# Optimization experiments

Hardware: AMD Instinct MI355X
Metric: run time of the kernel (lower is better)

The kernel has to match this reference:

```python
import jax, jax.numpy as jnp
import numpy as np

# arch config (matches init_kwargs)
T = 8
G = 16
D = 64
GG = G * G
THR = 0.5            # arch.object_threshold
Z_COS_MATCH_W = 5.0  # arch.z_cos_match_weight
ADJ_W = 1.0
PRES_W = 1.0
POOL_W = 1.0
OBJ_W = 10.0
FLOW_W = 1.0
FULL_OBJ = 200000.0  # arch.full_object_weight
FLOW_END = 100000.0  # arch.flow_cooling_end_step


def setup_inputs() -> dict:
    key = jax.random.key(0)
    k1, k2, k3 = jax.random.split(key, 3)
    B = 128
    return {
        "z_what": jax.random.normal(k1, (T * B, GG, D), dtype=jnp.float32),
        "z_pres_prob": jax.random.uniform(k2, (T * B, GG, 1), dtype=jnp.float32),
        "grid_flow": jax.random.uniform(k3, (T * B, GG, 1), dtype=jnp.float32),
        "global_step": 50000,
    }


def _maxpool3x3(x):
    # x: (N, C, G, G); torch MaxPool2d(3, stride=1, padding=1) pads with -inf
    return jax.lax.reduce_window(
        x, -jnp.inf, jax.lax.max,
        window_dimensions=(1, 1, 3, 3), window_strides=(1, 1, 1, 1),
        padding=[(0, 0), (0, 0), (1, 1), (1, 1)])


def reference(z_what, z_pres_prob, grid_flow, global_step):
    B = z_what.shape[0] // T
    zw = z_what.reshape(T, B, GG, D)
    zp = z_pres_prob.reshape(T, B, GG, 1)

    # ---- z_what_loss_grid_cell: adjacent squared deltas ----
    z_what_loss = jnp.sum((zw[1:] - zw[:-1]) ** 2)

    # ---- z_pres_loss_grid_cell ----
    sim = 1.0 - (zp[2:] - zp[:-2]) ** 2
    deltas = (zp[2:] - zp[1:-1]) ** 2 + (zp[:-2] - zp[1:-1]) ** 2
    z_pres_loss = jnp.sum(sim * deltas)

    # ---- z_what_consistency_pool (cosine_sim branch) ----
    w = jnp.abs(zw) * zp                                    # (T,B,GG,D)
    wi = w.transpose(0, 1, 3, 2).reshape(T * B, D, G, G)
    smoothed = _maxpool3x3(wi).reshape(T, B, D, GG).transpose(0, 1, 3, 2)
    dot = jnp.sum(smoothed[:-1] * w[1:], axis=-1)           # (T-1,B,GG)
    na = jnp.maximum(jnp.sqrt(jnp.sum(smoothed[:-1] ** 2, -1)), 1e-6)
    nb = jnp.maximum(jnp.sqrt(jnp.sum(w[1:] ** 2, -1)), 1e-6)
    cos_pool = dot / (na * nb)
    pw = zp[..., 0]
    pw = (pw[:-1] + pw[1:]) * 0.5                           # (T-1,B,GG)
    z_what_loss_pool = -jnp.sum(cos_pool * pw)

    # ---- z_what_consistency_objects (vectorized over objects) ----
    # For every active cell (t,b,i,j) at time t<T-1, compare its z_what (prior)
    # with z_what at t+1 over the 3x3 circular neighborhood, restricted to
    # neighbor cells whose z_pres > threshold. Loss per object:
    #   -z_cos_match_weight * max(sim) + sum(sim); skipped if no active neighbor.
    zpg = zp.reshape(T, B, G, G)
    zwg = zw.reshape(T, B, G, G, D)
    prior = zwg[:-1]                                        # (T-1,B,G,G,D)
    prior_n = jnp.maximum(jnp.sqrt(jnp.sum(prior ** 2, -1)), 1e-8)
    pres_prior = zpg[:-1] > THR                             # (T-1,B,G,G)
    sum_sim = jnp.zeros(prior.shape[:-1], dtype=prior.dtype)
    max_sim = jnp.full(prior.shape[:-1], -jnp.inf, dtype=prior.dtype)
    has_nb = jnp.zeros(prior.shape[:-1], dtype=bool)
    for di in (-1, 0, 1):
        for dj in (-1, 0, 1):
            nbw = jnp.roll(zwg[1:], (-di, -dj), axis=(2, 3))       # circular
            nbp = jnp.roll(zpg[1:], (-di, -dj), axis=(2, 3)) > THR
            dotn = jnp.sum(prior * nbw, axis=-1)
            nn = jnp.maximum(jnp.sqrt(jnp.sum(nbw ** 2, -1)), 1e-8)
            s = dotn / (prior_n * nn)
            sum_sim = sum_sim + jnp.where(nbp, s, 0.0)
            max_sim = jnp.maximum(max_sim, jnp.where(nbp, s, -jnp.inf))
            has_nb = has_nb | nbp
    valid = pres_prior & has_nb
    contrib = jnp.where(valid, -Z_COS_MATCH_W * max_sim + sum_sim, 0.0)
    z_what_loss_objects = jnp.sum(contrib)
    objects_detected = jnp.sum(pres_prior.astype(jnp.int32))

    # ---- compute_flow_loss ----
    zp_img = z_pres_prob.reshape(-1, 1, G, G)
    zp_max = _maxpool3x3(zp_img).reshape(-1, GG, 1)
    flow = grid_flow.reshape(-1, GG, 1)
    fmask = flow > 0.5
    flow_loss = jnp.sum(jnp.where(fmask, (zp_max - flow) ** 2, 0.0)) \
        + 100.0 * jnp.maximum(0.0, jnp.sum(zp_img) - jnp.sum(flow))

    # ---- total (Space base loss excluded; external submodule) ----
    scale_obj = min(1.0, float(global_step) / FULL_OBJ)
    scale_flow = max(0.0, 1.0 - float(global_step) / FLOW_END)
    loss = (z_what_loss * ADJ_W
            + z_pres_loss * PRES_W
            + z_what_loss_pool * POOL_W
            + z_what_loss_objects * scale_obj * OBJ_W
            + flow_loss * FLOW_W * scale_flow)
    return loss
```

## Files before the change

kernel.cpp:

```cpp
#include <hip/hip_runtime.h>
#include <math.h>

#define TT 8
#define BB 128
#define GG 256
#define DD 64
#define NCH 4
#define CF4 4
#define ST 5
#define NPAIR ((TT - 1) * BB)


__device__ inline float wred(float v) {
#pragma unroll
    for (int off = 32; off > 0; off >>= 1) v += __shfl_xor(v, off, 64);
    return v;
}
__device__ inline float dot4(float4 a, float4 b) {
    return a.x * b.x + a.y * b.y + a.z * b.z + a.w * b.w;
}
__device__ inline float4 fabs4(float4 a) {
    return make_float4(fabsf(a.x), fabsf(a.y), fabsf(a.z), fabsf(a.w));
}
__device__ inline float4 max4(float4 a, float4 b) {
    return make_float4(fmaxf(a.x, b.x), fmaxf(a.y, b.y), fmaxf(a.z, b.z), fmaxf(a.w, b.w));
}
__device__ inline float4 scale4(float4 a, float s) {
    return make_float4(a.x * s, a.y * s, a.z * s, a.w * s);
}
__device__ inline float4 sub4(float4 a, float4 b) {
    return make_float4(a.x - b.x, a.y - b.y, a.z - b.z, a.w - b.w);
}
__device__ inline float4 shfl4(float4 v, int src) {
    return make_float4(__shfl(v.x, src, 64), __shfl(v.y, src, 64),
                       __shfl(v.z, src, 64), __shfl(v.w, src, 64));
}

__global__ __launch_bounds__(256) void pair_kernel(const float* __restrict__ zw,
                                                   const float* __restrict__ zp,
                                                   const float* __restrict__ flow,
                                                   float* __restrict__ part) {
    const int pairIdx = blockIdx.x;
    const int t = pairIdx >> 7;
    const int b = pairIdx & (BB - 1);
    const int tid = threadIdx.x;
    const int gi = tid >> 4, gj = tid & 15;
    const int lane = tid & 63;

    __shared__ float4 shB[GG * ST];
    __shared__ float4 shR[GG * ST];
    __shared__ float pA[GG], pB[GG], nB[GG];
    __shared__ float bred[8][4];

    const float4* gA = (const float4*)zw + (size_t)(t * BB + b) * 1024;
    const float4* gB = gA + (size_t)BB * 1024;

    const float pAc = zp[(size_t)(t * BB + b) * GG + tid];
    const float pBc = zp[(size_t)((t + 1) * BB + b) * GG + tid];
    const float f = flow[(size_t)(t * BB + b) * GG + tid];
    float f7 = 0.f, pC = 0.f;
    if (t == 6) f7 = flow[(size_t)(7 * BB + b) * GG + tid];
    if (t <= 5) pC = zp[(size_t)((t + 2) * BB + b) * GG + tid];
    pA[tid] = pAc;
    pB[tid] = pBc;

    int nbc[9];
    unsigned inbM = 0;
    {
        int m = 0;
#pragma unroll
        for (int di = -1; di <= 1; di++) {
#pragma unroll
            for (int dj = -1; dj <= 1; dj++) {
                nbc[m] = (((gi + di) & 15) << 4) | ((gj + dj) & 15);
                if (((unsigned)(gi + di) < 16u) && ((unsigned)(gj + dj) < 16u))
                    inbM |= (1u << m);
                m++;
            }
        }
    }

    float zdiff = 0.f, sa = 0.f, sb = 0.f, poolDot = 0.f, poolN = 0.f;
    float dots[9] = {0.f, 0.f, 0.f, 0.f, 0.f, 0.f, 0.f, 0.f, 0.f};

    float4 cA[CF4], cB[CF4];
#pragma unroll
    for (int q = 0; q < CF4; q++) {
        cA[q] = gA[tid * 16 + q];
        cB[q] = gB[tid * 16 + q];
    }

#pragma unroll 1
    for (int c = 0; c < NCH; c++) {
        float4 nA4[CF4], nB4[CF4];
        if (c + 1 < NCH) {
#pragma unroll
            for (int q = 0; q < CF4; q++) {
                nA4[q] = gA[tid * 16 + (c + 1) * CF4 + q];
                nB4[q] = gB[tid * 16 + (c + 1) * CF4 + q];
            }
        }

#pragma unroll
        for (int q = 0; q < CF4; q++) {
            float4 d = sub4(cB[q], cA[q]);
            zdiff += dot4(d, d);
            sa += dot4(cA[q], cA[q]);
            sb += dot4(cB[q], cB[q]);
            dots[4] += dot4(cA[q], cB[q]);
            float4 wa = scale4(fabs4(cA[q]), pAc);
            float4 rm = wa;
            float4 lft = shfl4(wa, lane - 1);
            if (gj > 0) rm = max4(rm, lft);
            float4 rgt = shfl4(wa, lane + 1);
            if (gj < 15) rm = max4(rm, rgt);
            shB[tid * ST + q] = cB[q];
            shR[tid * ST + q] = rm;
        }
        __syncthreads();

#pragma unroll
        for (int k = 0; k < 9; k++) {
            if (k == 4) continue;
            int base = nbc[k] * ST;
#pragma unroll
            for (int q = 0; q < CF4; q++) dots[k] += dot4(cA[q], shB[base + q]);
        }
#pragma unroll
        for (int q = 0; q < CF4; q++) {
            float4 sm = shR[tid * ST + q];
            if (gi > 0) sm = max4(sm, shR[(tid - 16) * ST + q]);
            if (gi < 15) sm = max4(sm, shR[(tid + 16) * ST + q]);
            poolDot += dot4(sm, fabs4(cB[q]));
            poolN += dot4(sm, sm);
        }
        __syncthreads();

        if (c + 1 < NCH) {
#pragma unroll
            for (int q = 0; q < CF4; q++) { cA[q] = nA4[q]; cB[q] = nB4[q]; }
        }
    }

    nB[tid] = sqrtf(sb);
    __syncthreads();

    float prior_n = fmaxf(sqrtf(sa), 1e-8f);
    float sum_sim = 0.f, max_sim = -1e30f;
    bool has = false;
#pragma unroll
    for (int k = 0; k < 9; k++) {
        float nn = fmaxf(nB[nbc[k]], 1e-8f);
        float s = dots[k] / (prior_n * nn);
        if (pB[nbc[k]] > 0.5f) {
            sum_sim += s;
            max_sim = fmaxf(max_sim, s);
            has = true;
        }
    }
    float obj = ((pAc > 0.5f) && has) ? (sum_sim - 5.0f * max_sim) : 0.f;

    float na_pool = fmaxf(sqrtf(poolN), 1e-6f);
    float nb_pool = fmaxf(pBc * sqrtf(sb), 1e-6f);
    float poolc = -(pBc * poolDot) / (na_pool * nb_pool) * 0.5f * (pAc + pBc);

    float mx = pAc;
#pragma unroll
    for (int k = 0; k < 9; k++)
        if (k != 4 && ((inbM >> k) & 1u)) mx = fmaxf(mx, pA[nbc[k]]);
    float fsq = 0.f;
    if (f > 0.5f) { float d = mx - f; fsq = d * d; }
    float szp = pAc, sflow = f;
    if (t == 6) {
        float mxB = pBc;
#pragma unroll
        for (int k = 0; k < 9; k++)
            if (k != 4 && ((inbM >> k) & 1u)) mxB = fmaxf(mxB, pB[nbc[k]]);
        if (f7 > 0.5f) { float d = mxB - f7; fsq += d * d; }
        szp += pBc;
        sflow += f7;
    }

    float pres = 0.f;
    if (t <= 5) {
        float s02 = pC - pAc;
        float sim = 1.f - s02 * s02;
        float d2 = pC - pBc, d0 = pAc - pBc;
        pres = sim * (d2 * d2 + d0 * d0);
    }

    float r[7] = {zdiff, pres, poolc, obj, fsq, szp, sflow};
    int w = tid >> 6;
#pragma unroll
    for (int j = 0; j < 7; j++) {
        float rv = wred(r[j]);
        if (lane == 0) bred[j][w] = rv;
    }
    __syncthreads();
    if (tid < 7)
        part[pairIdx * 8 + tid] = bred[tid][0] + bred[tid][1] + bred[tid][2] + bred[tid][3];
}

__global__ __launch_bounds__(256) void final_kernel(const float* __restrict__ part,
                                                    const int* __restrict__ gs,
                                                    float* __restrict__ out) {
    const int tid = threadIdx.x;
    __shared__ float bred[7][4];
    float c[7] = {0.f, 0.f, 0.f, 0.f, 0.f, 0.f, 0.f};
    for (int p = tid; p < NPAIR; p += 256) {
        const float* r = part + p * 8;
#pragma unroll
        for (int j = 0; j < 7; j++) c[j] += r[j];
    }
    int w = tid >> 6, lane = tid & 63;
#pragma unroll
    for (int j = 0; j < 7; j++) {
        float rv = wred(c[j]);
        if (lane == 0) bred[j][w] = rv;
    }
    __syncthreads();
    if (tid == 0) {
        float s[7];
#pragma unroll
        for (int j = 0; j < 7; j++) s[j] = bred[j][0] + bred[j][1] + bred[j][2] + bred[j][3];
        float step = (float)gs[0];
        float scale_obj = fminf(1.f, step / 200000.f);
        float scale_flow = fmaxf(0.f, 1.f - step / 100000.f);
        float flow_loss = s[4] + 100.f * fmaxf(0.f, s[5] - s[6]);
        out[0] = s[0]
               + s[1]
               + s[2]
               + s[3] * scale_obj * 10.0f
               + flow_loss * scale_flow;
    }
}

extern "C" void kernel_launch(void* const* d_in, const int* in_sizes, int n_in,
                              void* d_out, int out_size, void* d_ws, size_t ws_size,
                              hipStream_t stream) {
    const float* zw = (const float*)d_in[0];
    const float* zp = (const float*)d_in[1];
    const float* fl = (const float*)d_in[2];
    const int* gs = (const int*)d_in[3];
    float* ws = (float*)d_ws;

    pair_kernel<<<NPAIR, 256, 0, stream>>>(zw, zp, fl, ws);
    final_kernel<<<1, 256, 0, stream>>>(ws, gs, (float*)d_out);
}
```

Measured before the change: 158.2 us.

## Split each frame pair into two half-grid blocks with halo rows

Each (t,b) pair is now handled by two 128-thread blocks, each covering 8 grid rows plus two halo rows. Halo threads reload the neighbouring rows' z_what and recompute their row-max and norms. One shared buffer is reused for the B features and the pool row-max, which adds an extra barrier per chunk. The register prefetch of the next chunk is dropped. The aim is more, smaller blocks and lower shared memory per block for better occupancy, at the cost of about 25% redundant halo loads and more synchronisation.

```diff
diff --git a/kernel.cpp b/kernel.cpp
--- a/kernel.cpp
+++ b/kernel.cpp
@@ -9,6 +9,8 @@
 #define CF4 4
 #define ST 5
 #define NPAIR ((TT - 1) * BB)
+#define NBLK (NPAIR * 2)
+#define LROWS 10
 
 
 __device__ inline float wred(float v) {
@@ -36,35 +38,53 @@
                        __shfl(v.z, src, 64), __shfl(v.w, src, 64));
 }
 
-__global__ __launch_bounds__(256) void pair_kernel(const float* __restrict__ zw,
+__global__ __launch_bounds__(128) void pair_kernel(const float* __restrict__ zw,
                                                    const float* __restrict__ zp,
                                                    const float* __restrict__ flow,
                                                    float* __restrict__ part) {
-    const int pairIdx = blockIdx.x;
+    const int blk = blockIdx.x;
+    const int pairIdx = blk >> 1;
+    const int half = blk & 1;
     const int t = pairIdx >> 7;
     const int b = pairIdx & (BB - 1);
+    const int r0 = half << 3;
     const int tid = threadIdx.x;
-    const int gi = tid >> 4, gj = tid & 15;
+    const int gj = tid & 15;
+    const int grow = r0 + (tid >> 4);
+    const int lr = (tid >> 4) + 1;
+    const int cell = (grow << 4) | gj;
     const int lane = tid & 63;
 
-    __shared__ float4 shB[GG * ST];
-    __shared__ float4 shR[GG * ST];
-    __shared__ float pA[GG], pB[GG], nB[GG];
-    __shared__ float bred[8][4];
+    const bool isHalo = (tid < 32);
+    const int hs = (tid < 16) ? 0 : 9;
+    const int hrow = (r0 - 1 + hs) & 15;
+    const int hcell = (hrow << 4) | gj;
+
+    __shared__ float4 shS[LROWS * 16 * ST];
+    __shared__ float pAloc[LROWS * 16], pBloc[LROWS * 16], nBloc[LROWS * 16];
+    __shared__ float bred[7][2];
 
     const float4* gA = (const float4*)zw + (size_t)(t * BB + b) * 1024;
     const float4* gB = gA + (size_t)BB * 1024;
-
-    const float pAc = zp[(size_t)(t * BB + b) * GG + tid];
-    const float pBc = zp[(size_t)((t + 1) * BB + b) * GG + tid];
-    const float f = flow[(size_t)(t * BB + b) * GG + tid];
+    const float* zpA = zp + (size_t)(t * BB + b) * GG;
+    const float* zpB = zp + (size_t)((t + 1) * BB + b) * GG;
+
+    const float pAc = zpA[cell];
+    const float pBc = zpB[cell];
+    pAloc[lr * 16 + gj] = pAc;
+    pBloc[lr * 16 + gj] = pBc;
+    float pAh = 0.f;
+    if (isHalo) {
+        pAh = zpA[hcell];
+        pAloc[hs * 16 + gj] = pAh;
+        pBloc[hs * 16 + gj] = zpB[hcell];
+    }
+    const float f = flow[(size_t)(t * BB + b) * GG + cell];
     float f7 = 0.f, pC = 0.f;
-    if (t == 6) f7 = flow[(size_t)(7 * BB + b) * GG + tid];
-    if (t <= 5) pC = zp[(size_t)((t + 2) * BB + b) * GG + tid];
-    pA[tid] = pAc;
-    pB[tid] = pBc;
-
-    int nbc[9];
+    if (t == 6) f7 = flow[(size_t)(7 * BB + b) * GG + cell];
+    if (t <= 5) pC = zp[(size_t)((t + 2) * BB + b) * GG + cell];
+
+    int nbl[9];
     unsigned inbM = 0;
     {
         int m = 0;
@@ -72,35 +92,41 @@
         for (int di = -1; di <= 1; di++) {
 #pragma unroll
             for (int dj = -1; dj <= 1; dj++) {
-                nbc[m] = (((gi + di) & 15) << 4) | ((gj + dj) & 15);
-                if (((unsigned)(gi + di) < 16u) && ((unsigned)(gj + dj) < 16u))
+                nbl[m] = (lr + di) * 16 + ((gj + dj) & 15);
+                if (((unsigned)(grow + di) < 16u) && ((unsigned)(gj + dj) < 16u))
                     inbM |= (1u << m);
                 m++;
             }
         }
     }
-
-    float zdiff = 0.f, sa = 0.f, sb = 0.f, poolDot = 0.f, poolN = 0.f;
+    __syncthreads();
+
+    float zdiff = 0.f, sa = 0.f, sb = 0.f, hsb = 0.f, poolDot = 0.f, poolN = 0.f;
     float dots[9] = {0.f, 0.f, 0.f, 0.f, 0.f, 0.f, 0.f, 0.f, 0.f};
-
-    float4 cA[CF4], cB[CF4];
-#pragma unroll
-    for (int q = 0; q < CF4; q++) {
-        cA[q] = gA[tid * 16 + q];
-        cB[q] = gB[tid * 16 + q];
-    }
 
 #pragma unroll 1
     for (int c = 0; c < NCH; c++) {
-        float4 nA4[CF4], nB4[CF4];
-        if (c + 1 < NCH) {
+        float4 cA[CF4], cB[CF4], rm[CF4], hrm[CF4];
+#pragma unroll
+        for (int q = 0; q < CF4; q++) {
+            cA[q] = gA[cell * 16 + c * CF4 + q];
+            cB[q] = gB[cell * 16 + c * CF4 + q];
+        }
+        float4 hB4[CF4];
+        if (isHalo) {
 #pragma unroll
             for (int q = 0; q < CF4; q++) {
-                nA4[q] = gA[tid * 16 + (c + 1) * CF4 + q];
-                nB4[q] = gB[tid * 16 + (c + 1) * CF4 + q];
+                float4 hA4 = gA[hcell * 16 + c * CF4 + q];
+                hB4[q] = gB[hcell * 16 + c * CF4 + q];
+                hsb += dot4(hB4[q], hB4[q]);
+                float4 wa = scale4(fabs4(hA4), pAh);
+                hrm[q] = wa;
+                float4 lft = shfl4(wa, lane - 1);
+                if (gj > 0) hrm[q] = max4(hrm[q], lft);
+                float4 rgt = shfl4(wa, lane + 1);
+                if (gj < 15) hrm[q] = max4(hrm[q], rgt);
             }
         }
-
 #pragma unroll
         for (int q = 0; q < CF4; q++) {
             float4 d = sub4(cB[q], cA[q]);
@@ -109,40 +135,50 @@
             sb += dot4(cB[q], cB[q]);
             dots[4] += dot4(cA[q], cB[q]);
             float4 wa = scale4(fabs4(cA[q]), pAc);
-            float4 rm = wa;
+            rm[q] = wa;
             float4 lft = shfl4(wa, lane - 1);
-            if (gj > 0) rm = max4(rm, lft);
+            if (gj > 0) rm[q] = max4(rm[q], lft);
             float4 rgt = shfl4(wa, lane + 1);
-            if (gj < 15) rm = max4(rm, rgt);
-            shB[tid * ST + q] = cB[q];
-            shR[tid * ST + q] = rm;
+            if (gj < 15) rm[q] = max4(rm[q], rgt);
+            shS[(lr * 16 + gj) * ST + q] = cB[q];
+        }
+        if (isHalo) {
+#pragma unroll
+            for (int q = 0; q < CF4; q++) shS[(hs * 16 + gj) * ST + q] = hB4[q];
         }
         __syncthreads();
 
 #pragma unroll
         for (int k = 0; k < 9; k++) {
             if (k == 4) continue;
-            int base = nbc[k] * ST;
-#pragma unroll
-            for (int q = 0; q < CF4; q++) dots[k] += dot4(cA[q], shB[base + q]);
-        }
+            int base = nbl[k] * ST;
+#pragma unroll
+            for (int q = 0; q < CF4; q++) dots[k] += dot4(cA[q], shS[base + q]);
+        }
+        __syncthreads();
+
+#pragma unroll
+        for (int q = 0; q < CF4; q++) shS[(lr * 16 + gj) * ST + q] = rm[q];
+        if (isHalo) {
+#pragma unroll
+            for (int q = 0; q < CF4; q++) shS[(hs * 16 + gj) * ST + q] = hrm[q];
+        }
+        __syncthreads();
+
+        const bool up = (grow > 0), dn = (grow < 15);
 #pragma unroll
         for (int q = 0; q < CF4; q++) {
-            float4 sm = shR[tid * ST + q];
-            if (gi > 0) sm = max4(sm, shR[(tid - 16) * ST + q]);
-            if (gi < 15) sm = max4(sm, shR[(tid + 16) * ST + q]);
+            float4 sm = rm[q];
+            if (up) sm = max4(sm, shS[((lr - 1) * 16 + gj) * ST + q]);
+            if (dn) sm = max4(sm, shS[((lr + 1) * 16 + gj) * ST + q]);
             poolDot += dot4(sm, fabs4(cB[q]));
             poolN += dot4(sm, sm);
         }
         __syncthreads();
-
-        if (c + 1 < NCH) {
-#pragma unroll
-            for (int q = 0; q < CF4; q++) { cA[q] = nA4[q]; cB[q] = nB4[q]; }
-        }
-    }
-
-    nB[tid] = sqrtf(sb);
+    }
+
+    nBloc[lr * 16 + gj] = sqrtf(sb);
+    if (isHalo) nBloc[hs * 16 + gj] = sqrtf(hsb);
     __syncthreads();
 
     float prior_n = fmaxf(sqrtf(sa), 1e-8f);
@@ -150,9 +186,9 @@
     bool has = false;
 #pragma unroll
     for (int k = 0; k < 9; k++) {
-        float nn = fmaxf(nB[nbc[k]], 1e-8f);
+        float nn = fmaxf(nBloc[nbl[k]], 1e-8f);
         float s = dots[k] / (prior_n * nn);
-        if (pB[nbc[k]] > 0.5f) {
+        if (pBloc[nbl[k]] > 0.5f) {
             sum_sim += s;
             max_sim = fmaxf(max_sim, s);
             has = true;
@@ -167,7 +203,7 @@
     float mx = pAc;
 #pragma unroll
     for (int k = 0; k < 9; k++)
-        if (k != 4 && ((inbM >> k) & 1u)) mx = fmaxf(mx, pA[nbc[k]]);
+        if (k != 4 && ((inbM >> k) & 1u)) mx = fmaxf(mx, pAloc[nbl[k]]);
     float fsq = 0.f;
     if (f > 0.5f) { float d = mx - f; fsq = d * d; }
     float szp = pAc, sflow = f;
@@ -175,7 +211,7 @@
         float mxB = pBc;
 #pragma unroll
         for (int k = 0; k < 9; k++)
-            if (k != 4 && ((inbM >> k) & 1u)) mxB = fmaxf(mxB, pB[nbc[k]]);
+            if (k != 4 && ((inbM >> k) & 1u)) mxB = fmaxf(mxB, pBloc[nbl[k]]);
         if (f7 > 0.5f) { float d = mxB - f7; fsq += d * d; }
         szp += pBc;
         sflow += f7;
@@ -198,7 +234,7 @@
     }
     __syncthreads();
     if (tid < 7)
-        part[pairIdx * 8 + tid] = bred[tid][0] + bred[tid][1] + bred[tid][2] + bred[tid][3];
+        part[blk * 8 + tid] = bred[tid][0] + bred[tid][1];
 }
 
 __global__ __launch_bounds__(256) void final_kernel(const float* __restrict__ part,
@@ -207,7 +243,7 @@
     const int tid = threadIdx.x;
     __shared__ float bred[7][4];
     float c[7] = {0.f, 0.f, 0.f, 0.f, 0.f, 0.f, 0.f};
-    for (int p = tid; p < NPAIR; p += 256) {
+    for (int p = tid; p < NBLK; p += 256) {
         const float* r = part + p * 8;
 #pragma unroll
         for (int j = 0; j < 7; j++) c[j] += r[j];
@@ -244,6 +280,6 @@
     const int* gs = (const int*)d_in[3];
     float* ws = (float*)d_ws;
 
-    pair_kernel<<<NPAIR, 256, 0, stream>>>(zw, zp, fl, ws);
+    pair_kernel<<<NBLK, 128, 0, stream>>>(zw, zp, fl, ws);
     final_kernel<<<1, 256, 0, stream>>>(ws, gs, (float*)d_out);
 }
```

New measurement: 177.2 us. 12.0% more time.
